# Optimization experiments

Measured on AMD Instinct MI355X. Metric: run time of the kernel, lower is better.

The kernel has to match this reference:

```python
import jax, jax.numpy as jnp
import numpy as np

B, V, R, D, E = 4, 50000, 64, 64, 500000


def setup_inputs() -> dict:
    key = jax.random.key(0)
    ks = jax.random.split(key, 10)
    x = jax.random.normal(ks[0], (B, V, D), dtype=jnp.float32)
    z = jax.random.normal(ks[1], (B, R, D), dtype=jnp.float32)
    h = jax.random.randint(ks[2], (E,), 0, V)
    r = jax.random.randint(ks[3], (E,), 0, R)
    t = jax.random.randint(ks[4], (E,), 0, V)
    edge_index = jnp.stack([h, r, t], axis=1)  # (E, 3) triples (head, rel, tail)
    s = 1.0 / np.sqrt(D)
    W1 = jax.random.normal(ks[5], (D, D), dtype=jnp.float32) * s
    b1 = jnp.zeros((D,), dtype=jnp.float32)
    W2 = jax.random.normal(ks[6], (D, D), dtype=jnp.float32) * s
    b2 = jnp.zeros((D,), dtype=jnp.float32)
    alpha = jax.random.normal(ks[7], (1, D), dtype=jnp.float32)
    gamma = jnp.ones((D,), dtype=jnp.float32)
    beta = jnp.zeros((D,), dtype=jnp.float32)
    return {"x": x, "z": z, "edge_index": edge_index, "W1": W1, "b1": b1,
            "W2": W2, "b2": b2, "alpha": alpha, "gamma": gamma, "beta": beta}


def _layernorm(h, gamma, beta, eps=1e-5):
    mu = jnp.mean(h, axis=-1, keepdims=True)
    var = jnp.mean((h - mu) ** 2, axis=-1, keepdims=True)
    return (h - mu) * jax.lax.rsqrt(var + eps) * gamma + beta


def reference(x, z, edge_index, W1, b1, W2, b2, alpha, gamma, beta):
    b, v, d = x.shape
    dst = edge_index[:, 0]   # row index of sparse matrix (head)
    etype = edge_index[:, 1]  # relation type
    src = edge_index[:, 2]   # column index (tail)
    # split: 'b l d -> l (b d)'
    xf = jnp.transpose(x, (1, 0, 2)).reshape(v, b * d)          # (V, B*D)
    zf = jnp.transpose(z, (1, 0, 2)).reshape(z.shape[1], b * d)  # (R, B*D)
    # generalized_rspmm: gather, elementwise multiply (edge_weight == 1), scatter-add
    msg = zf[etype] * xf[src]                                   # (E, B*D)
    agg = jax.ops.segment_sum(msg, dst, num_segments=v)         # (V, B*D)
    # merge: 'l (b d) -> b l d'
    out = jnp.transpose(agg.reshape(v, b, d), (1, 0, 2))        # (B, V, D)
    h = out + alpha * x
    h = jnp.maximum(h @ W1 + b1, 0.0) @ W2 + b2                 # MLP: Linear-ReLU-Linear
    h = _layernorm(h, gamma, beta)
    return h + x
```

## Files before the change

kernel.cpp:

```cpp
#include <hip/hip_runtime.h>

#define Bdim 4
#define Vdim 50000
#define Rdim 64
#define Ddim 64
#define Edim 500000
#define CAP 64
#define NV 16
#define AST 68
#define H2ST 68

typedef __attribute__((ext_vector_type(8))) short short8;
typedef __attribute__((ext_vector_type(4))) short short4v;
typedef __attribute__((ext_vector_type(4))) float float4v;

static __device__ __forceinline__ unsigned short f2bf(float f) {
    unsigned u = __float_as_uint(f);
    u += 0x7FFF + ((u >> 16) & 1);
    return (unsigned short)(u >> 16);
}
static __device__ __forceinline__ float bf2f(unsigned short h) {
    return __uint_as_float(((unsigned)h) << 16);
}

__global__ __launch_bounds__(256) void bucket_kernel(
    const int* __restrict__ ei, int* __restrict__ cursor,
    unsigned* __restrict__ bucket)
{
    int e = blockIdx.x * 256 + threadIdx.x;
    if (e >= Edim) return;
    int dst = ei[e * 3 + 0];
    int et  = ei[e * 3 + 1];
    int src = ei[e * 3 + 2];
    int pos = atomicAdd(&cursor[dst], 1);
    if (pos < CAP) bucket[dst * CAP + pos] = ((unsigned)et << 16) | (unsigned)src;
}

__global__ __launch_bounds__(256, 5) void fused_kernel(
    const float* __restrict__ x,
    const float* __restrict__ z,
    const int*   __restrict__ cursor,
    const unsigned* __restrict__ bucket,
    const float* __restrict__ W1, const float* __restrict__ b1,
    const float* __restrict__ W2, const float* __restrict__ b2,
    const float* __restrict__ alpha, const float* __restrict__ gamma,
    const float* __restrict__ beta,
    float* __restrict__ out)
{
    __shared__ __align__(16) unsigned short pool[2 * 64 * AST];
    __shared__ __align__(16) unsigned short wh[64 * AST];
    __shared__ __align__(16) float vecs[5 * 64];
    __shared__ __align__(16) unsigned bkt[NV * CAP];

    unsigned short* ah = pool;
    unsigned short* al = pool + 64 * AST;
    float* h2s = (float*)pool;

    int tid = threadIdx.x;
    int v0 = blockIdx.x * NV;

    for (int i = tid; i < 4096; i += 256) {
        int k = i >> 6, n = i & 63;
        wh[n * AST + k] = f2bf(W1[i]);
    }
    for (int i = tid; i < NV * CAP; i += 256) bkt[i] = bucket[v0 * CAP + i];
    if (tid < 64) {
        vecs[tid      ] = b1[tid];
        vecs[tid + 64 ] = b2[tid];
        vecs[tid + 128] = alpha[tid];
        vecs[tid + 192] = gamma[tid];
        vecs[tid + 256] = beta[tid];
    }
    __syncthreads();

    int w    = tid >> 6;
    int lane = tid & 63;

    {
        int b  = lane >> 4;
        int d4 = (lane & 15) * 4;
        const float4 av = *(const float4*)&vecs[128 + d4];

        int vbase = v0 + w * 4;
        int cn[4];
        #pragma unroll
        for (int q = 0; q < 4; ++q) {
            int c = cursor[vbase + q];
            cn[q] = c < CAP ? c : CAP;
        }
        int n = max(max(cn[0], cn[1]), max(cn[2], cn[3]));

        float4 acc[4];
        #pragma unroll
        for (int q = 0; q < 4; ++q) acc[q] = make_float4(0.f, 0.f, 0.f, 0.f);

        #pragma unroll
        for (int q = 0; q < 4; ++q) {
            const float4 xs = *(const float4*)(x + ((size_t)b * Vdim + vbase + q) * Ddim + d4);
            acc[q].x = fmaf(av.x, xs.x, acc[q].x);
            acc[q].y = fmaf(av.y, xs.y, acc[q].y);
            acc[q].z = fmaf(av.z, xs.z, acc[q].z);
            acc[q].w = fmaf(av.w, xs.w, acc[q].w);
        }

        for (int i = 0; i < n; i += 4) {
            unsigned p[16];
            float    m[16];
            #pragma unroll
            for (int u = 0; u < 4; ++u) {
                #pragma unroll
                for (int q = 0; q < 4; ++q) {
                    int idx = i + u;
                    unsigned praw = bkt[(w * 4 + q) * CAP + idx];
                    bool ok = idx < cn[q];
                    p[u * 4 + q] = ok ? praw : 0u;
                    m[u * 4 + q] = ok ? 1.f : 0.f;
                }
            }
            #pragma unroll
            for (int k = 0; k < 16; ++k) {
                int src = (int)(p[k] & 0xFFFFu);
                int et  = (int)(p[k] >> 16);
                const float4 xv = *(const float4*)(x + ((size_t)b * Vdim + src) * Ddim + d4);
                const float4 zv = *(const float4*)(z + ((size_t)b * Rdim + et ) * Ddim + d4);
                float mx = m[k];
                int q = k & 3;
                acc[q].x = fmaf(mx * xv.x, zv.x, acc[q].x);
                acc[q].y = fmaf(mx * xv.y, zv.y, acc[q].y);
                acc[q].z = fmaf(mx * xv.z, zv.z, acc[q].z);
                acc[q].w = fmaf(mx * xv.w, zv.w, acc[q].w);
            }
        }

        #pragma unroll
        for (int q = 0; q < 4; ++q) {
            int rr = (w * 4 + q) * 4 + b;
            short4v hi, lo;
            hi.x = (short)f2bf(acc[q].x); lo.x = (short)f2bf(acc[q].x - bf2f(hi.x));
            hi.y = (short)f2bf(acc[q].y); lo.y = (short)f2bf(acc[q].y - bf2f(hi.y));
            hi.z = (short)f2bf(acc[q].z); lo.z = (short)f2bf(acc[q].z - bf2f(hi.z));
            hi.w = (short)f2bf(acc[q].w); lo.w = (short)f2bf(acc[q].w - bf2f(hi.w));
            *(short4v*)&ah[rr * AST + d4] = hi;
            *(short4v*)&al[rr * AST + d4] = lo;
        }
    }
    __syncthreads();

    int quad = lane >> 4;
    int l15  = lane & 15;
    int mrow = w * 16 + l15;
    int koff = quad * 8;

    float4v acc2[4];

    {
        short8 aH0 = *(const short8*)&ah[mrow * AST + koff];
        short8 aH1 = *(const short8*)&ah[mrow * AST + 32 + koff];
        short8 aL0 = *(const short8*)&al[mrow * AST + koff];
        short8 aL1 = *(const short8*)&al[mrow * AST + 32 + koff];
        #pragma unroll
        for (int nt = 0; nt < 4; ++nt) {
            float bv = vecs[nt * 16 + l15];
            float4v c = {bv, bv, bv, bv};
            short8 b0 = *(const short8*)&wh[(nt * 16 + l15) * AST + koff];
            short8 b1f = *(const short8*)&wh[(nt * 16 + l15) * AST + 32 + koff];
            c = __builtin_amdgcn_mfma_f32_16x16x32_bf16(aH0, b0,  c, 0, 0, 0);
            c = __builtin_amdgcn_mfma_f32_16x16x32_bf16(aL0, b0,  c, 0, 0, 0);
            c = __builtin_amdgcn_mfma_f32_16x16x32_bf16(aH1, b1f, c, 0, 0, 0);
            c = __builtin_amdgcn_mfma_f32_16x16x32_bf16(aL1, b1f, c, 0, 0, 0);
            acc2[nt] = c;
        }
    }
    __syncthreads();

    #pragma unroll
    for (int nt = 0; nt < 4; ++nt) {
        #pragma unroll
        for (int r = 0; r < 4; ++r) {
            float v = fmaxf(acc2[nt][r], 0.0f);
            int row = w * 16 + quad * 4 + r;
            int col = nt * 16 + l15;
            unsigned short h = f2bf(v);
            ah[row * AST + col] = h;
            al[row * AST + col] = f2bf(v - bf2f(h));
        }
    }
    for (int i = tid; i < 4096; i += 256) {
        int k = i >> 6, n = i & 63;
        wh[n * AST + k] = f2bf(W2[i]);
    }
    __syncthreads();

    {
        short8 aH0 = *(const short8*)&ah[mrow * AST + koff];
        short8 aH1 = *(const short8*)&ah[mrow * AST + 32 + koff];
        short8 aL0 = *(const short8*)&al[mrow * AST + koff];
        short8 aL1 = *(const short8*)&al[mrow * AST + 32 + koff];
        #pragma unroll
        for (int nt = 0; nt < 4; ++nt) {
            float bv = vecs[64 + nt * 16 + l15];
            float4v c = {bv, bv, bv, bv};
            short8 b0 = *(const short8*)&wh[(nt * 16 + l15) * AST + koff];
            short8 b1f = *(const short8*)&wh[(nt * 16 + l15) * AST + 32 + koff];
            c = __builtin_amdgcn_mfma_f32_16x16x32_bf16(aH0, b0,  c, 0, 0, 0);
            c = __builtin_amdgcn_mfma_f32_16x16x32_bf16(aL0, b0,  c, 0, 0, 0);
            c = __builtin_amdgcn_mfma_f32_16x16x32_bf16(aH1, b1f, c, 0, 0, 0);
            c = __builtin_amdgcn_mfma_f32_16x16x32_bf16(aL1, b1f, c, 0, 0, 0);
            acc2[nt] = c;
        }
    }
    __syncthreads();

    #pragma unroll
    for (int nt = 0; nt < 4; ++nt) {
        #pragma unroll
        for (int r = 0; r < 4; ++r) {
            int row = w * 16 + quad * 4 + r;
            int col = nt * 16 + l15;
            h2s[row * H2ST + col] = acc2[nt][r];
        }
    }
    __syncthreads();

    {
        float ga = vecs[192 + lane];
        float be = vecs[256 + lane];
        for (int r = 0; r < 16; ++r) {
            int rr = w * 16 + r;
            float val = h2s[rr * H2ST + lane];

            float s = val;
            #pragma unroll
            for (int off = 32; off >= 1; off >>= 1) s += __shfl_xor(s, off);
            float mu = s * (1.0f / 64.0f);
            float diff = val - mu;
            float q = diff * diff;
            #pragma unroll
            for (int off = 32; off >= 1; off >>= 1) q += __shfl_xor(q, off);
            float ynorm = diff * rsqrtf(q * (1.0f / 64.0f) + 1e-5f);

            int v = v0 + (rr >> 2);
            int b = rr & 3;
            size_t base = ((size_t)b * Vdim + v) * Ddim;
            float xj = x[base + lane];
            out[base + lane] = fmaf(ynorm, ga, be) + xj;
        }
    }
}

extern "C" void kernel_launch(void* const* d_in, const int* in_sizes, int n_in,
                              void* d_out, int out_size, void* d_ws, size_t ws_size,
                              hipStream_t stream) {
    const float* x     = (const float*)d_in[0];
    const float* z     = (const float*)d_in[1];
    const int*   ei    = (const int*)  d_in[2];
    const float* W1    = (const float*)d_in[3];
    const float* b1    = (const float*)d_in[4];
    const float* W2    = (const float*)d_in[5];
    const float* b2    = (const float*)d_in[6];
    const float* alpha = (const float*)d_in[7];
    const float* gamma = (const float*)d_in[8];
    const float* beta  = (const float*)d_in[9];
    float* out = (float*)d_out;

    int* cursor      = (int*)d_ws;
    unsigned* bucket = (unsigned*)(cursor + Vdim);

    hipMemsetAsync(cursor, 0, (size_t)Vdim * sizeof(int), stream);

    int blocksE = (Edim + 255) / 256;
    bucket_kernel<<<blocksE, 256, 0, stream>>>(ei, cursor, bucket);

    fused_kernel<<<Vdim / NV, 256, 0, stream>>>(x, z, cursor, bucket,
                                                W1, b1, W2, b2,
                                                alpha, gamma, beta, out);
}
```

Baseline: 271.2 us.

## Shrink block tile to 4 vertices with one vertex per wave and per-wave MFMA column tile

Each block now handles 4 vertices instead of 16. Each wave gathers edges for a single vertex, and in the MLP each wave computes one 16-column tile of a 16-row MFMA instead of four tiles over its own rows. Shared memory per block shrinks and the launch bound rises to 8 blocks per SM, so more blocks and waves can be resident for latency hiding in the irregular gather. In exchange, W1/W2 are converted and staged into LDS 4x more often overall, and each wave has less memory-level parallelism inside its gather loop.

```diff
diff --git a/kernel.cpp b/kernel.cpp
--- a/kernel.cpp
+++ b/kernel.cpp
@@ -6,7 +6,7 @@
 #define Ddim 64
 #define Edim 500000
 #define CAP 64
-#define NV 16
+#define NV 4
 #define AST 68
 #define H2ST 68
 
@@ -36,7 +36,7 @@
     if (pos < CAP) bucket[dst * CAP + pos] = ((unsigned)et << 16) | (unsigned)src;
 }
 
-__global__ __launch_bounds__(256, 5) void fused_kernel(
+__global__ __launch_bounds__(256, 8) void fused_kernel(
     const float* __restrict__ x,
     const float* __restrict__ z,
     const int*   __restrict__ cursor,
@@ -47,13 +47,13 @@
     const float* __restrict__ beta,
     float* __restrict__ out)
 {
-    __shared__ __align__(16) unsigned short pool[2 * 64 * AST];
+    __shared__ __align__(16) unsigned short pool[2 * 16 * AST];
     __shared__ __align__(16) unsigned short wh[64 * AST];
     __shared__ __align__(16) float vecs[5 * 64];
     __shared__ __align__(16) unsigned bkt[NV * CAP];
 
     unsigned short* ah = pool;
-    unsigned short* al = pool + 64 * AST;
+    unsigned short* al = pool + 16 * AST;
     float* h2s = (float*)pool;
 
     int tid = threadIdx.x;
@@ -63,7 +63,7 @@
         int k = i >> 6, n = i & 63;
         wh[n * AST + k] = f2bf(W1[i]);
     }
-    for (int i = tid; i < NV * CAP; i += 256) bkt[i] = bucket[v0 * CAP + i];
+    bkt[tid] = bucket[v0 * CAP + tid];
     if (tid < 64) {
         vecs[tid      ] = b1[tid];
         vecs[tid + 64 ] = b2[tid];
@@ -75,71 +75,57 @@
 
     int w    = tid >> 6;
     int lane = tid & 63;
-
-    {
-        int b  = lane >> 4;
-        int d4 = (lane & 15) * 4;
+    int b    = lane >> 4;
+    int d4   = (lane & 15) * 4;
+
+    {
         const float4 av = *(const float4*)&vecs[128 + d4];
-
-        int vbase = v0 + w * 4;
-        int cn[4];
-        #pragma unroll
-        for (int q = 0; q < 4; ++q) {
-            int c = cursor[vbase + q];
-            cn[q] = c < CAP ? c : CAP;
-        }
-        int n = max(max(cn[0], cn[1]), max(cn[2], cn[3]));
-
-        float4 acc[4];
-        #pragma unroll
-        for (int q = 0; q < 4; ++q) acc[q] = make_float4(0.f, 0.f, 0.f, 0.f);
-
-        #pragma unroll
-        for (int q = 0; q < 4; ++q) {
-            const float4 xs = *(const float4*)(x + ((size_t)b * Vdim + vbase + q) * Ddim + d4);
-            acc[q].x = fmaf(av.x, xs.x, acc[q].x);
-            acc[q].y = fmaf(av.y, xs.y, acc[q].y);
-            acc[q].z = fmaf(av.z, xs.z, acc[q].z);
-            acc[q].w = fmaf(av.w, xs.w, acc[q].w);
-        }
-
-        for (int i = 0; i < n; i += 4) {
-            unsigned p[16];
-            float    m[16];
+        int v = v0 + w;
+        int c = cursor[v];
+        int cn = c < CAP ? c : CAP;
+
+        float4 acc;
+        {
+            const float4 xs = *(const float4*)(x + ((size_t)b * Vdim + v) * Ddim + d4);
+            acc.x = av.x * xs.x;
+            acc.y = av.y * xs.y;
+            acc.z = av.z * xs.z;
+            acc.w = av.w * xs.w;
+        }
+
+        for (int i = 0; i < cn; i += 4) {
+            unsigned p[4];
+            float    m[4];
             #pragma unroll
             for (int u = 0; u < 4; ++u) {
-                #pragma unroll
-                for (int q = 0; q < 4; ++q) {
-                    int idx = i + u;
-                    unsigned praw = bkt[(w * 4 + q) * CAP + idx];
-                    bool ok = idx < cn[q];
-                    p[u * 4 + q] = ok ? praw : 0u;
-                    m[u * 4 + q] = ok ? 1.f : 0.f;
-                }
+                int idx = i + u;
+                bool ok = idx < cn;
+                int idxc = ok ? idx : 0;
+                unsigned praw = bkt[w * CAP + idxc];
+                p[u] = ok ? praw : 0u;
+                m[u] = ok ? 1.f : 0.f;
             }
             #pragma unroll
-            for (int k = 0; k < 16; ++k) {
-                int src = (int)(p[k] & 0xFFFFu);
-                int et  = (int)(p[k] >> 16);
+            for (int u = 0; u < 4; ++u) {
+                int src = (int)(p[u] & 0xFFFFu);
+                int et  = (int)(p[u] >> 16);
                 const float4 xv = *(const float4*)(x + ((size_t)b * Vdim + src) * Ddim + d4);
                 const float4 zv = *(const float4*)(z + ((size_t)b * Rdim + et ) * Ddim + d4);
-                float mx = m[k];
-                int q = k & 3;
-                acc[q].x = fmaf(mx * xv.x, zv.x, acc[q].x);
-                acc[q].y = fmaf(mx * xv.y, zv.y, acc[q].y);
-                acc[q].z = fmaf(mx * xv.z, zv.z, acc[q].z);
-                acc[q].w = fmaf(mx * xv.w, zv.w, acc[q].w);
+                float mx = m[u];
+                acc.x = fmaf(mx * xv.x, zv.x, acc.x);
+                acc.y = fmaf(mx * xv.y, zv.y, acc.y);
+                acc.z = fmaf(mx * xv.z, zv.z, acc.z);
+                acc.w = fmaf(mx * xv.w, zv.w, acc.w);
             }
         }
 
-        #pragma unroll
-        for (int q = 0; q < 4; ++q) {
-            int rr = (w * 4 + q) * 4 + b;
+        {
+            int rr = w * 4 + b;
             short4v hi, lo;
-            hi.x = (short)f2bf(acc[q].x); lo.x = (short)f2bf(acc[q].x - bf2f(hi.x));
-            hi.y = (short)f2bf(acc[q].y); lo.y = (short)f2bf(acc[q].y - bf2f(hi.y));
-            hi.z = (short)f2bf(acc[q].z); lo.z = (short)f2bf(acc[q].z - bf2f(hi.z));
-            hi.w = (short)f2bf(acc[q].w); lo.w = (short)f2bf(acc[q].w - bf2f(hi.w));
+            hi.x = (short)f2bf(acc.x); lo.x = (short)f2bf(acc.x - bf2f(hi.x));
+            hi.y = (short)f2bf(acc.y); lo.y = (short)f2bf(acc.y - bf2f(hi.y));
+            hi.z = (short)f2bf(acc.z); lo.z = (short)f2bf(acc.z - bf2f(hi.z));
+            hi.w = (short)f2bf(acc.w); lo.w = (short)f2bf(acc.w - bf2f(hi.w));
             *(short4v*)&ah[rr * AST + d4] = hi;
             *(short4v*)&al[rr * AST + d4] = lo;
         }
@@ -148,42 +134,36 @@
 
     int quad = lane >> 4;
     int l15  = lane & 15;
-    int mrow = w * 16 + l15;
     int koff = quad * 8;
-
-    float4v acc2[4];
-
-    {
-        short8 aH0 = *(const short8*)&ah[mrow * AST + koff];
-        short8 aH1 = *(const short8*)&ah[mrow * AST + 32 + koff];
-        short8 aL0 = *(const short8*)&al[mrow * AST + koff];
-        short8 aL1 = *(const short8*)&al[mrow * AST + 32 + koff];
-        #pragma unroll
-        for (int nt = 0; nt < 4; ++nt) {
-            float bv = vecs[nt * 16 + l15];
-            float4v c = {bv, bv, bv, bv};
-            short8 b0 = *(const short8*)&wh[(nt * 16 + l15) * AST + koff];
-            short8 b1f = *(const short8*)&wh[(nt * 16 + l15) * AST + 32 + koff];
-            c = __builtin_amdgcn_mfma_f32_16x16x32_bf16(aH0, b0,  c, 0, 0, 0);
-            c = __builtin_amdgcn_mfma_f32_16x16x32_bf16(aL0, b0,  c, 0, 0, 0);
-            c = __builtin_amdgcn_mfma_f32_16x16x32_bf16(aH1, b1f, c, 0, 0, 0);
-            c = __builtin_amdgcn_mfma_f32_16x16x32_bf16(aL1, b1f, c, 0, 0, 0);
-            acc2[nt] = c;
-        }
+    int nt   = w;
+
+    float4v acc2;
+
+    {
+        short8 aH0 = *(const short8*)&ah[l15 * AST + koff];
+        short8 aH1 = *(const short8*)&ah[l15 * AST + 32 + koff];
+        short8 aL0 = *(const short8*)&al[l15 * AST + koff];
+        short8 aL1 = *(const short8*)&al[l15 * AST + 32 + koff];
+        float bv = vecs[nt * 16 + l15];
+        float4v c = {bv, bv, bv, bv};
+        short8 b0  = *(const short8*)&wh[(nt * 16 + l15) * AST + koff];
+        short8 b1f = *(const short8*)&wh[(nt * 16 + l15) * AST + 32 + koff];
+        c = __builtin_amdgcn_mfma_f32_16x16x32_bf16(aH0, b0,  c, 0, 0, 0);
+        c = __builtin_amdgcn_mfma_f32_16x16x32_bf16(aL0, b0,  c, 0, 0, 0);
+        c = __builtin_amdgcn_mfma_f32_16x16x32_bf16(aH1, b1f, c, 0, 0, 0);
+        c = __builtin_amdgcn_mfma_f32_16x16x32_bf16(aL1, b1f, c, 0, 0, 0);
+        acc2 = c;
     }
     __syncthreads();
 
     #pragma unroll
-    for (int nt = 0; nt < 4; ++nt) {
-        #pragma unroll
-        for (int r = 0; r < 4; ++r) {
-            float v = fmaxf(acc2[nt][r], 0.0f);
-            int row = w * 16 + quad * 4 + r;
-            int col = nt * 16 + l15;
-            unsigned short h = f2bf(v);
-            ah[row * AST + col] = h;
-            al[row * AST + col] = f2bf(v - bf2f(h));
-        }
+    for (int r = 0; r < 4; ++r) {
+        float v = fmaxf(acc2[r], 0.0f);
+        int row = quad * 4 + r;
+        int col = nt * 16 + l15;
+        unsigned short h = f2bf(v);
+        ah[row * AST + col] = h;
+        al[row * AST + col] = f2bf(v - bf2f(h));
     }
     for (int i = tid; i < 4096; i += 256) {
         int k = i >> 6, n = i & 63;
@@ -192,41 +172,36 @@
     __syncthreads();
 
     {
-        short8 aH0 = *(const short8*)&ah[mrow * AST + koff];
-        short8 aH1 = *(const short8*)&ah[mrow * AST + 32 + koff];
-        short8 aL0 = *(const short8*)&al[mrow * AST + koff];
-        short8 aL1 = *(const short8*)&al[mrow * AST + 32 + koff];
-        #pragma unroll
-        for (int nt = 0; nt < 4; ++nt) {
-            float bv = vecs[64 + nt * 16 + l15];
-            float4v c = {bv, bv, bv, bv};
-            short8 b0 = *(const short8*)&wh[(nt * 16 + l15) * AST + koff];
-            short8 b1f = *(const short8*)&wh[(nt * 16 + l15) * AST + 32 + koff];
-            c = __builtin_amdgcn_mfma_f32_16x16x32_bf16(aH0, b0,  c, 0, 0, 0);
-            c = __builtin_amdgcn_mfma_f32_16x16x32_bf16(aL0, b0,  c, 0, 0, 0);
-            c = __builtin_amdgcn_mfma_f32_16x16x32_bf16(aH1, b1f, c, 0, 0, 0);
-            c = __builtin_amdgcn_mfma_f32_16x16x32_bf16(aL1, b1f, c, 0, 0, 0);
-            acc2[nt] = c;
-        }
+        short8 aH0 = *(const short8*)&ah[l15 * AST + koff];
+        short8 aH1 = *(const short8*)&ah[l15 * AST + 32 + koff];
+        short8 aL0 = *(const short8*)&al[l15 * AST + koff];
+        short8 aL1 = *(const short8*)&al[l15 * AST + 32 + koff];
+        float bv = vecs[64 + nt * 16 + l15];
+        float4v c = {bv, bv, bv, bv};
+        short8 b0  = *(const short8*)&wh[(nt * 16 + l15) * AST + koff];
+        short8 b1f = *(const short8*)&wh[(nt * 16 + l15) * AST + 32 + koff];
+        c = __builtin_amdgcn_mfma_f32_16x16x32_bf16(aH0, b0,  c, 0, 0, 0);
+        c = __builtin_amdgcn_mfma_f32_16x16x32_bf16(aL0, b0,  c, 0, 0, 0);
+        c = __builtin_amdgcn_mfma_f32_16x16x32_bf16(aH1, b1f, c, 0, 0, 0);
+        c = __builtin_amdgcn_mfma_f32_16x16x32_bf16(aL1, b1f, c, 0, 0, 0);
+        acc2 = c;
     }
     __syncthreads();
 
     #pragma unroll
-    for (int nt = 0; nt < 4; ++nt) {
+    for (int r = 0; r < 4; ++r) {
+        int row = quad * 4 + r;
+        int col = nt * 16 + l15;
+        h2s[row * H2ST + col] = acc2[r];
+    }
+    __syncthreads();
+
+    {
+        float ga = vecs[192 + lane];
+        float be = vecs[256 + lane];
         #pragma unroll
         for (int r = 0; r < 4; ++r) {
-            int row = w * 16 + quad * 4 + r;
-            int col = nt * 16 + l15;
-            h2s[row * H2ST + col] = acc2[nt][r];
-        }
-    }
-    __syncthreads();
-
-    {
-        float ga = vecs[192 + lane];
-        float be = vecs[256 + lane];
-        for (int r = 0; r < 16; ++r) {
-            int rr = w * 16 + r;
+            int rr = w * 4 + r;
             float val = h2s[rr * H2ST + lane];
 
             float s = val;
@@ -239,9 +214,9 @@
             for (int off = 32; off >= 1; off >>= 1) q += __shfl_xor(q, off);
             float ynorm = diff * rsqrtf(q * (1.0f / 64.0f) + 1e-5f);
 
-            int v = v0 + (rr >> 2);
-            int b = rr & 3;
-            size_t base = ((size_t)b * Vdim + v) * Ddim;
+            int v = v0 + w;
+            int bb = rr & 3;
+            size_t base = ((size_t)bb * Vdim + v) * Ddim;
             float xj = x[base + lane];
             out[base + lane] = fmaf(ynorm, ga, be) + xj;
         }
```

New measurement: 249.6 us. 1.09x faster.
